# Kernel optimization log

Hardware: AMD Instinct MI355X
Metric: run time of the kernel (lower is better)

The kernel has to match this reference:

```python
import jax, jax.numpy as jnp
import numpy as np

N = 50000
E = 800000
IN_DIM = 128
OUT_DIM = 128


def setup_inputs() -> dict:
    key = jax.random.key(0)
    k_x, k_e, k_w, k_b = jax.random.split(key, 4)
    x = jax.random.normal(k_x, (N, IN_DIM), dtype=jnp.float32)
    edge_index = jax.random.randint(k_e, (2, E), 0, N, dtype=jnp.int64)
    # nn.Linear(in_dim, out_dim): W [out, in], b [out], uniform(-1/sqrt(in), 1/sqrt(in))
    bound = 1.0 / np.sqrt(IN_DIM)
    W = jax.random.uniform(k_w, (OUT_DIM, IN_DIM), jnp.float32, -bound, bound)
    b = jax.random.uniform(k_b, (OUT_DIM,), jnp.float32, -bound, bound)
    return {"x": x, "edge_index": edge_index, "W": W, "b": b}


def reference(x, edge_index, W, b):
    row, col = edge_index[0], edge_index[1]
    n = x.shape[0]
    # degree of destination nodes (count of incoming edges per node)
    deg = jax.ops.segment_sum(jnp.ones_like(col, dtype=x.dtype), col, num_segments=n)
    deg_inv = jnp.where(deg > 0, 1.0 / deg, 0.0)  # 1/0 -> 0, as in torch code
    norm = deg_inv[col]  # [E]
    msg = x[row] * norm[:, None]  # [E, in_dim]
    out = jax.ops.segment_sum(msg, col, num_segments=n)  # mean of neighbors
    h = x - out  # high-pass filter
    return jax.nn.relu(h @ W.T + b)
```

## Files before the change

### kernel.cpp

```cpp
#include <hip/hip_runtime.h>
#include <hip/hip_bf16.h>

#define DIM 128
#define NB 512
#define BCAP 2048
#define PART_CH 2048
#define SPLIT 4

typedef __attribute__((ext_vector_type(8))) short bf16x8;
typedef __attribute__((ext_vector_type(4))) float f32x4;

struct PartS { int lh[NB]; int lbase[NB]; };
struct GemmS { unsigned short Wt[64][132]; unsigned short xs[64][132]; };

__global__ __launch_bounds__(256) void k_partgemm(const int* __restrict__ ei,
                                                  const float* __restrict__ x,
                                                  const float* __restrict__ W,
                                                  int* __restrict__ gcur,
                                                  unsigned* __restrict__ ebuf,
                                                  unsigned short* __restrict__ yb,
                                                  int nE, int cpb, int PB, int nN) {
    __shared__ union { PartS p; GemmS g; } sm;
    int t = threadIdx.x;

    if ((int)blockIdx.x >= PB) {
        int n0 = ((int)blockIdx.x - PB) * 64;
        #define B16(f) (__hip_bfloat16_raw(__float2bfloat16(f)).x)
        for (int i = t; i < 64 * DIM / 4; i += 256) {
            int r = i >> 5, k = (i & 31) * 4;
            int n = n0 + r;
            float4 v = make_float4(0.f, 0.f, 0.f, 0.f);
            if (n < nN) v = ((const float4*)x)[(size_t)n * 32 + (i & 31)];
            sm.g.xs[r][k] = B16(v.x); sm.g.xs[r][k + 1] = B16(v.y);
            sm.g.xs[r][k + 2] = B16(v.z); sm.g.xs[r][k + 3] = B16(v.w);
        }
        __syncthreads();

        int wv = t >> 6, l = t & 63;
        int lr = l & 15, lg = l >> 4;
        int row0 = wv * 16;

        bf16x8 af[4];
        #pragma unroll
        for (int kt = 0; kt < 4; ++kt)
            af[kt] = *(const bf16x8*)&sm.g.xs[row0 + lr][kt * 32 + lg * 8];

        #pragma unroll
        for (int ch = 0; ch < 2; ++ch) {
            if (ch) __syncthreads();
            for (int i = t; i < 64 * DIM / 4; i += 256) {
                int o = i >> 5, k = (i & 31) * 4;
                float4 v = ((const float4*)W)[(size_t)(ch * 64 + o) * 32 + (i & 31)];
                sm.g.Wt[o][k] = B16(v.x); sm.g.Wt[o][k + 1] = B16(v.y);
                sm.g.Wt[o][k + 2] = B16(v.z); sm.g.Wt[o][k + 3] = B16(v.w);
            }
            __syncthreads();

            #pragma unroll
            for (int ot = 0; ot < 4; ++ot) {
                f32x4 acc = {0.f, 0.f, 0.f, 0.f};
                #pragma unroll
                for (int kt = 0; kt < 4; ++kt) {
                    bf16x8 bf = *(const bf16x8*)&sm.g.Wt[ot * 16 + lr][kt * 32 + lg * 8];
                    acc = __builtin_amdgcn_mfma_f32_16x16x32_bf16(af[kt], bf, acc, 0, 0, 0);
                }
                int o = ch * 64 + ot * 16 + lr;
                #pragma unroll
                for (int j = 0; j < 4; ++j) {
                    int n = n0 + row0 + lg * 4 + j;
                    if (n < nN)
                        yb[(size_t)n * DIM + o] = B16(acc[j]);
                }
            }
        }
        #undef B16
        return;
    }

    int base = blockIdx.x * PART_CH;
    for (int i = t; i < NB; i += 256) sm.p.lh[i] = 0;
    __syncthreads();
    unsigned pk[8];
    int bk[8], rk[8];
    #pragma unroll
    for (int k = 0; k < 8; ++k) {
        int e = base + k * 256 + t;
        if (e < nE) {
            int row = ei[e];
            int col = ei[nE + e];
            int b = (int)((unsigned)col / (unsigned)cpb);
            bk[k] = b;
            pk[k] = ((unsigned)row << 16) | (unsigned)(col - b * cpb);
            rk[k] = atomicAdd(&sm.p.lh[b], 1);
        } else bk[k] = -1;
    }
    __syncthreads();
    for (int i = t; i < NB; i += 256) {
        int c = sm.p.lh[i];
        sm.p.lbase[i] = c ? atomicAdd(&gcur[i], c) : 0;
    }
    __syncthreads();
    #pragma unroll
    for (int k = 0; k < 8; ++k) {
        if (bk[k] >= 0) {
            int pos = sm.p.lbase[bk[k]] + rk[k];
            if (pos < BCAP) ebuf[(size_t)bk[k] * BCAP + pos] = pk[k];
        }
    }
}

__global__ __launch_bounds__(256) void k_gather(const unsigned short* __restrict__ yb,
                                                const unsigned* __restrict__ ebuf,
                                                const int* __restrict__ gcur,
                                                const float* __restrict__ bias,
                                                float* __restrict__ out,
                                                int nN, int cpb) {
    __shared__ unsigned short rowlist[BCAP];
    __shared__ int chist[128];
    __shared__ int cstart[128];
    __shared__ int part[256];
    int b = blockIdx.x / SPLIT;
    int q = blockIdx.x % SPLIT;
    int t = threadIdx.x;
    int c0 = b * cpb;
    int ncols = min(cpb, nN - c0);
    if (ncols <= 0) return;
    int CQ = (cpb + SPLIT - 1) / SPLIT;
    int mylo = q * CQ;
    int myhi = min(mylo + CQ, ncols);
    if (mylo >= ncols) return;
    int ne = min(gcur[b], BCAP);

    if (t < 128) chist[t] = 0;
    __syncthreads();

    unsigned ed[8];
    int rk[8];
    #pragma unroll
    for (int k = 0; k < 8; ++k) {
        int i = k * 256 + t;
        ed[k] = (i < ne) ? ebuf[(size_t)b * BCAP + i] : 0xFFFFFFFFu;
        if (ed[k] != 0xFFFFFFFFu) rk[k] = atomicAdd(&chist[ed[k] & 0xFFFF], 1);
    }
    __syncthreads();

    int v = (t < 128) ? chist[t] : 0;
    part[t] = v;
    __syncthreads();
    for (int off = 1; off < 128; off <<= 1) {
        int add = (t >= off) ? part[t - off] : 0;
        __syncthreads();
        part[t] += add;
        __syncthreads();
    }
    if (t < 128) cstart[t] = part[t] - v;
    __syncthreads();

    #pragma unroll
    for (int k = 0; k < 8; ++k) {
        if (ed[k] != 0xFFFFFFFFu)
            rowlist[cstart[ed[k] & 0xFFFF] + rk[k]] = (unsigned short)(ed[k] >> 16);
    }
    __syncthreads();

    int l = t & 31;
    const ushort4* yb4 = (const ushort4*)yb;
    float4 bv = ((const float4*)bias)[l];
    #define BF2F(u) __uint_as_float(((unsigned)(u)) << 16)
    #define ACC(vv) { a0 += BF2F(vv.x); a1 += BF2F(vv.y); a2 += BF2F(vv.z); a3 += BF2F(vv.w); }
    for (int cc = mylo + (t >> 5); cc < myhi; cc += 8) {
        int cdeg = chist[cc];
        int sb = cstart[cc];
        float a0 = 0.f, a1 = 0.f, a2 = 0.f, a3 = 0.f;
        int j = 0;
        for (; j + 8 <= cdeg; j += 8) {
            int r0 = rowlist[sb + j],     r1 = rowlist[sb + j + 1];
            int r2 = rowlist[sb + j + 2], r3 = rowlist[sb + j + 3];
            int r4 = rowlist[sb + j + 4], r5 = rowlist[sb + j + 5];
            int r6 = rowlist[sb + j + 6], r7 = rowlist[sb + j + 7];
            ushort4 v0 = yb4[(size_t)r0 * 32 + l];
            ushort4 v1 = yb4[(size_t)r1 * 32 + l];
            ushort4 v2 = yb4[(size_t)r2 * 32 + l];
            ushort4 v3 = yb4[(size_t)r3 * 32 + l];
            ushort4 v4 = yb4[(size_t)r4 * 32 + l];
            ushort4 v5 = yb4[(size_t)r5 * 32 + l];
            ushort4 v6 = yb4[(size_t)r6 * 32 + l];
            ushort4 v7 = yb4[(size_t)r7 * 32 + l];
            ACC(v0) ACC(v1) ACC(v2) ACC(v3) ACC(v4) ACC(v5) ACC(v6) ACC(v7)
        }
        for (; j < cdeg; ++j) {
            ushort4 vv = yb4[(size_t)rowlist[sb + j] * 32 + l];
            ACC(vv)
        }
        float dinv = cdeg > 0 ? 1.0f / (float)cdeg : 0.0f;
        int n = c0 + cc;
        ushort4 sv = yb4[(size_t)n * 32 + l];
        float4 o;
        o.x = fmaxf(BF2F(sv.x) - dinv * a0 + bv.x, 0.f);
        o.y = fmaxf(BF2F(sv.y) - dinv * a1 + bv.y, 0.f);
        o.z = fmaxf(BF2F(sv.z) - dinv * a2 + bv.z, 0.f);
        o.w = fmaxf(BF2F(sv.w) - dinv * a3 + bv.w, 0.f);
        ((float4*)out)[(size_t)n * 32 + l] = o;
    }
    #undef ACC
    #undef BF2F
}

extern "C" void kernel_launch(void* const* d_in, const int* in_sizes, int n_in,
                              void* d_out, int out_size, void* d_ws, size_t ws_size,
                              hipStream_t stream) {
    const float* x = (const float*)d_in[0];
    const int* ei = (const int*)d_in[1];
    const float* W = (const float*)d_in[2];
    const float* b = (const float*)d_in[3];
    float* out = (float*)d_out;

    int nN = in_sizes[0] / DIM;
    int nE = in_sizes[1] / 2;

    int* gcur = (int*)d_ws;
    unsigned* ebuf = (unsigned*)(gcur + NB);
    unsigned short* yb = (unsigned short*)(ebuf + (size_t)NB * BCAP);

    int cpb = (nN + NB - 1) / NB;
    int nbuckets = (nN + cpb - 1) / cpb;

    (void)hipMemsetAsync(gcur, 0, NB * sizeof(int), stream);

    int PB = (nE + PART_CH - 1) / PART_CH;
    int GB = (nN + 63) / 64;
    k_partgemm<<<PB + GB, 256, 0, stream>>>(ei, x, W, gcur, ebuf, yb, nE, cpb, PB, nN);

    k_gather<<<nbuckets * SPLIT, 256, 0, stream>>>(yb, ebuf, gcur, b, out, nN, cpb);
}
```

Baseline: 69.59 us.

## Split gather into a CSR-build kernel and a flat per-node gather kernel

Moves the per-bucket column sort (histogram, scan, scatter) out of the gather kernel into a separate k_csr kernel, which writes global rowlists, start offsets and degrees. The gather kernel then assigns one 32-lane group to each node across a flat grid. The old SPLIT scheme repeated the bucket sort four times per bucket and limited parallelism to those bucket blocks. The cost is an extra kernel launch plus a global round trip for the rowlist and offset arrays.

```diff
diff --git a/kernel.cpp b/kernel.cpp
--- a/kernel.cpp
+++ b/kernel.cpp
@@ -5,7 +5,6 @@
 #define NB 512
 #define BCAP 2048
 #define PART_CH 2048
-#define SPLIT 4
 
 typedef __attribute__((ext_vector_type(8))) short bf16x8;
 typedef __attribute__((ext_vector_type(4))) float f32x4;
@@ -109,26 +108,20 @@
     }
 }
 
-__global__ __launch_bounds__(256) void k_gather(const unsigned short* __restrict__ yb,
-                                                const unsigned* __restrict__ ebuf,
-                                                const int* __restrict__ gcur,
-                                                const float* __restrict__ bias,
-                                                float* __restrict__ out,
-                                                int nN, int cpb) {
-    __shared__ unsigned short rowlist[BCAP];
+__global__ __launch_bounds__(256) void k_csr(const unsigned* __restrict__ ebuf,
+                                             const int* __restrict__ gcur,
+                                             unsigned short* __restrict__ rowlist16,
+                                             int* __restrict__ cstartg,
+                                             int* __restrict__ cdegg,
+                                             int nN, int cpb) {
     __shared__ int chist[128];
     __shared__ int cstart[128];
     __shared__ int part[256];
-    int b = blockIdx.x / SPLIT;
-    int q = blockIdx.x % SPLIT;
+    int b = blockIdx.x;
     int t = threadIdx.x;
     int c0 = b * cpb;
     int ncols = min(cpb, nN - c0);
     if (ncols <= 0) return;
-    int CQ = (cpb + SPLIT - 1) / SPLIT;
-    int mylo = q * CQ;
-    int myhi = min(mylo + CQ, ncols);
-    if (mylo >= ncols) return;
     int ne = min(gcur[b], BCAP);
 
     if (t < 128) chist[t] = 0;
@@ -159,49 +152,61 @@
     #pragma unroll
     for (int k = 0; k < 8; ++k) {
         if (ed[k] != 0xFFFFFFFFu)
-            rowlist[cstart[ed[k] & 0xFFFF] + rk[k]] = (unsigned short)(ed[k] >> 16);
-    }
-    __syncthreads();
-
-    int l = t & 31;
+            rowlist16[(size_t)b * BCAP + cstart[ed[k] & 0xFFFF] + rk[k]] =
+                (unsigned short)(ed[k] >> 16);
+    }
+    if (t < ncols) {
+        cstartg[c0 + t] = b * BCAP + cstart[t];
+        cdegg[c0 + t] = chist[t];
+    }
+}
+
+__global__ __launch_bounds__(256) void k_gather(const unsigned short* __restrict__ yb,
+                                                const unsigned short* __restrict__ rowlist16,
+                                                const int* __restrict__ cstartg,
+                                                const int* __restrict__ cdegg,
+                                                const float* __restrict__ bias,
+                                                float* __restrict__ out,
+                                                int nN) {
+    int idx = blockIdx.x * 256 + threadIdx.x;
+    int g = idx >> 5;
+    int l = idx & 31;
+    if (g >= nN) return;
+    int s = cstartg[g];
+    int d = cdegg[g];
+    const unsigned short* lst = rowlist16 + s;
     const ushort4* yb4 = (const ushort4*)yb;
     float4 bv = ((const float4*)bias)[l];
+
+    float a0 = 0.f, a1 = 0.f, a2 = 0.f, a3 = 0.f;
     #define BF2F(u) __uint_as_float(((unsigned)(u)) << 16)
     #define ACC(vv) { a0 += BF2F(vv.x); a1 += BF2F(vv.y); a2 += BF2F(vv.z); a3 += BF2F(vv.w); }
-    for (int cc = mylo + (t >> 5); cc < myhi; cc += 8) {
-        int cdeg = chist[cc];
-        int sb = cstart[cc];
-        float a0 = 0.f, a1 = 0.f, a2 = 0.f, a3 = 0.f;
-        int j = 0;
-        for (; j + 8 <= cdeg; j += 8) {
-            int r0 = rowlist[sb + j],     r1 = rowlist[sb + j + 1];
-            int r2 = rowlist[sb + j + 2], r3 = rowlist[sb + j + 3];
-            int r4 = rowlist[sb + j + 4], r5 = rowlist[sb + j + 5];
-            int r6 = rowlist[sb + j + 6], r7 = rowlist[sb + j + 7];
-            ushort4 v0 = yb4[(size_t)r0 * 32 + l];
-            ushort4 v1 = yb4[(size_t)r1 * 32 + l];
-            ushort4 v2 = yb4[(size_t)r2 * 32 + l];
-            ushort4 v3 = yb4[(size_t)r3 * 32 + l];
-            ushort4 v4 = yb4[(size_t)r4 * 32 + l];
-            ushort4 v5 = yb4[(size_t)r5 * 32 + l];
-            ushort4 v6 = yb4[(size_t)r6 * 32 + l];
-            ushort4 v7 = yb4[(size_t)r7 * 32 + l];
-            ACC(v0) ACC(v1) ACC(v2) ACC(v3) ACC(v4) ACC(v5) ACC(v6) ACC(v7)
-        }
-        for (; j < cdeg; ++j) {
-            ushort4 vv = yb4[(size_t)rowlist[sb + j] * 32 + l];
-            ACC(vv)
-        }
-        float dinv = cdeg > 0 ? 1.0f / (float)cdeg : 0.0f;
-        int n = c0 + cc;
-        ushort4 sv = yb4[(size_t)n * 32 + l];
-        float4 o;
-        o.x = fmaxf(BF2F(sv.x) - dinv * a0 + bv.x, 0.f);
-        o.y = fmaxf(BF2F(sv.y) - dinv * a1 + bv.y, 0.f);
-        o.z = fmaxf(BF2F(sv.z) - dinv * a2 + bv.z, 0.f);
-        o.w = fmaxf(BF2F(sv.w) - dinv * a3 + bv.w, 0.f);
-        ((float4*)out)[(size_t)n * 32 + l] = o;
-    }
+    int j = 0;
+    for (; j + 8 <= d; j += 8) {
+        int r0 = lst[j],     r1 = lst[j + 1], r2 = lst[j + 2], r3 = lst[j + 3];
+        int r4 = lst[j + 4], r5 = lst[j + 5], r6 = lst[j + 6], r7 = lst[j + 7];
+        ushort4 v0 = yb4[(size_t)r0 * 32 + l];
+        ushort4 v1 = yb4[(size_t)r1 * 32 + l];
+        ushort4 v2 = yb4[(size_t)r2 * 32 + l];
+        ushort4 v3 = yb4[(size_t)r3 * 32 + l];
+        ushort4 v4 = yb4[(size_t)r4 * 32 + l];
+        ushort4 v5 = yb4[(size_t)r5 * 32 + l];
+        ushort4 v6 = yb4[(size_t)r6 * 32 + l];
+        ushort4 v7 = yb4[(size_t)r7 * 32 + l];
+        ACC(v0) ACC(v1) ACC(v2) ACC(v3) ACC(v4) ACC(v5) ACC(v6) ACC(v7)
+    }
+    for (; j < d; ++j) {
+        ushort4 vv = yb4[(size_t)lst[j] * 32 + l];
+        ACC(vv)
+    }
+    float dinv = d > 0 ? 1.0f / (float)d : 0.0f;
+    ushort4 sv = yb4[(size_t)g * 32 + l];
+    float4 o;
+    o.x = fmaxf(BF2F(sv.x) - dinv * a0 + bv.x, 0.f);
+    o.y = fmaxf(BF2F(sv.y) - dinv * a1 + bv.y, 0.f);
+    o.z = fmaxf(BF2F(sv.z) - dinv * a2 + bv.z, 0.f);
+    o.w = fmaxf(BF2F(sv.w) - dinv * a3 + bv.w, 0.f);
+    ((float4*)out)[(size_t)g * 32 + l] = o;
     #undef ACC
     #undef BF2F
 }
@@ -219,8 +224,11 @@
     int nE = in_sizes[1] / 2;
 
     int* gcur = (int*)d_ws;
-    unsigned* ebuf = (unsigned*)(gcur + NB);
-    unsigned short* yb = (unsigned short*)(ebuf + (size_t)NB * BCAP);
+    int* cstartg = gcur + NB;
+    int* cdegg = cstartg + nN;
+    unsigned* ebuf = (unsigned*)(cdegg + nN);
+    unsigned short* rowlist16 = (unsigned short*)(ebuf + (size_t)NB * BCAP);
+    unsigned short* yb = rowlist16 + (size_t)NB * BCAP;
 
     int cpb = (nN + NB - 1) / NB;
     int nbuckets = (nN + cpb - 1) / cpb;
@@ -231,5 +239,8 @@
     int GB = (nN + 63) / 64;
     k_partgemm<<<PB + GB, 256, 0, stream>>>(ei, x, W, gcur, ebuf, yb, nE, cpb, PB, nN);
 
-    k_gather<<<nbuckets * SPLIT, 256, 0, stream>>>(yb, ebuf, gcur, b, out, nN, cpb);
-}
+    k_csr<<<nbuckets, 256, 0, stream>>>(ebuf, gcur, rowlist16, cstartg, cdegg, nN, cpb);
+
+    int gb2 = (nN * 32 + 255) / 256;
+    k_gather<<<gb2, 256, 0, stream>>>(yb, rowlist16, cstartg, cdegg, b, out, nN);
+}
```

After: 75.44 us. 1.08x slower.
